# Kernel optimization log

Measured on AMD Instinct MI355X. Metric: run time of the kernel, lower is better.

Reference implementation:

```python
import jax, jax.numpy as jnp
import numpy as np

# ---- real Clebsch-Gordon tensors (Wigner 3j up to norm/sign) via equivariance null-space ----
def _su2_gens(l):
    m = np.arange(-l, l + 1)
    Lz = np.diag(m).astype(complex)
    c = np.sqrt(l * (l + 1) - m[:-1] * (m[:-1] + 1))
    Lp = np.zeros((2 * l + 1, 2 * l + 1), complex)
    Lp[np.arange(1, 2 * l + 1), np.arange(2 * l)] = c
    Lm = Lp.conj().T
    return (Lp + Lm) / 2, (Lp - Lm) / 2j, Lz

def _q_real(l):
    # complex -> real spherical-harmonic change of basis
    Q = np.zeros((2 * l + 1, 2 * l + 1), complex)
    s2 = np.sqrt(2.0)
    for m in range(-l, l + 1):
        i = m + l
        if m == 0:
            Q[i, l] = 1.0
        elif m > 0:
            Q[i, l + m] = (-1.0) ** m / s2
            Q[i, l - m] = 1.0 / s2
        else:
            Q[i, l + m] = 1j / s2
            Q[i, l - m] = -1j * (-1.0) ** m / s2
    return Q

def _real_gens(l):
    Q = _q_real(l)
    return [np.real(Q @ (1j * L) @ Q.conj().T) for L in _su2_gens(l)]

_CG = {}
def clebsch_gordon(l1, l2, l3):
    key = (l1, l2, l3)
    if key not in _CG:
        n1, n2, n3 = 2 * l1 + 1, 2 * l2 + 1, 2 * l3 + 1
        G = [_real_gens(l) for l in (l1, l2, l3)]
        rows = []
        for a in range(3):
            rows.append(np.kron(G[0][a], np.eye(n2 * n3))
                        + np.kron(np.eye(n1), np.kron(G[1][a], np.eye(n3)))
                        + np.kron(np.eye(n1 * n2), G[2][a]))
        _, s, Vh = np.linalg.svd(np.concatenate(rows, 0))
        v = Vh[-1]  # unique invariant vector (unit norm)
        if v[np.argmax(np.abs(v))] < 0:
            v = -v
        _CG[key] = v.reshape(n1, n2, n3).astype(np.float32)
    return _CG[key]

# ---- static irreps configuration (mul, degree l, parity p) ----
TP_L = [(32, 0, 1), (32, 1, -1)]
TP_R = [(32, 0, 1), (32, 1, -1)]
IRREPS_IN = [(128, 0, 1), (128, 1, -1), (128, 1, 1), (128, 2, 1)]
B = 8192
D_IN = sum(m * (2 * l + 1) for m, l, _ in IRREPS_IN)  # 1536

def _key(l, p):
    return f"{l}{'e' if p == 1 else 'o'}"

def _build_out_irreps():
    mul, order = {}, []
    for ml, ll, pl in TP_L:
        for mr, lr, pr in TP_R:
            p = pl * pr
            for l in range(abs(ll - lr), ll + lr + 1):
                k = _key(l, p)
                if k not in mul:
                    mul[k] = 0
                    order.append((l, p))
                mul[k] += ml * mr
    return [(mul[_key(l, p)], l, p) for (l, p) in order]

IRREPS_OUT = _build_out_irreps()  # [(2048,0,1),(2048,1,-1),(1024,1,1),(1024,2,1)]

def _build_schedule():
    # replicates the original's tail-consuming slice logic per (pair, output irrep)
    starts, off = [], 0
    for mul, l, p in IRREPS_OUT:
        starts.append(off)
        off += mul * (2 * l + 1)
    rem = {_key(l, p): mul for mul, l, p in IRREPS_OUT}
    sched = []
    for ml, ll, pl in TP_L:
        for mr, lr, pr in TP_R:
            mul = ml * mr
            terms = []
            for i, (mo, l, p) in enumerate(IRREPS_OUT):
                if p != pl * pr or not (abs(ll - lr) <= l <= ll + lr):
                    continue
                k = _key(l, p)
                stop = starts[i] + rem[k] * (2 * l + 1)
                start = stop - mul * (2 * l + 1)
                rem[k] -= mul
                terms.append((start, stop, l, clebsch_gordon(ll, lr, l)))
            sched.append((ml, ll, mr, lr, terms))
    assert all(v == 0 for v in rem.values())
    return sched, off

SCHEDULE, D_OUT = _build_schedule()  # D_OUT == 16384

def setup_inputs() -> dict:
    key = jax.random.key(0)
    ks = jax.random.split(key, 5)
    x = jax.random.normal(ks[0], (B, D_IN), jnp.float32)
    w_0e = jax.random.normal(ks[1], (128, 2048), jnp.float32) / np.sqrt(128.0)
    w_1o = jax.random.normal(ks[2], (128, 2048), jnp.float32) / np.sqrt(128.0)
    w_1e = jax.random.normal(ks[3], (128, 1024), jnp.float32) / np.sqrt(128.0)
    w_2e = jax.random.normal(ks[4], (128, 1024), jnp.float32) / np.sqrt(128.0)
    return {"x": x, "w_0e": w_0e, "w_1o": w_1o, "w_1e": w_1e, "w_2e": w_2e}

def _linear(x, ws):
    # e3nn-style PointwiseLinear: mix multiplicities within each irrep type
    in_off, off = {}, 0
    for m, l, p in IRREPS_IN:
        in_off[_key(l, p)] = (off, m)
        off += m * (2 * l + 1)
    outs = []
    for (mo, l, p), w in zip(IRREPS_OUT, ws):
        o, mi = in_off[_key(l, p)]
        d = 2 * l + 1
        xi = x[:, o:o + mi * d].reshape(-1, mi, d)  # [B, mul_in, 2l+1]
        yo = jnp.einsum('bui,uv->bvi', xi, w)       # [B, mul_out, 2l+1]
        outs.append(yo.reshape(xi.shape[0], mo * d))
    return jnp.concatenate(outs, axis=1)  # [B, D_OUT]

def reference(x, w_0e, w_1o, w_1e, w_2e):
    y = _linear(x, (w_0e, w_1o, w_1e, w_2e))
    blocks = []
    for ml, ll, mr, lr, terms in SCHEDULE:
        acc = None
        for start, stop, l, cg in terms:
            a = y[:, start:stop].reshape(-1, ml, mr, 2 * l + 1)  # [B,mul_l,mul_r,2l+1]
            t = jnp.einsum('bmni,lri->bmlnr', a, jnp.asarray(cg))
            acc = t if acc is None else acc + t  # [B,mul_l,2ll+1,mul_r,2lr+1]
        blocks.append(acc.reshape(acc.shape[0], -1))
    return jnp.concatenate(blocks, axis=1)  # [B, 16384]
```

## Files before the change

### kernel.cpp

```cpp
#include <hip/hip_runtime.h>


typedef __attribute__((ext_vector_type(8))) __bf16 bf16x8;
typedef __attribute__((ext_vector_type(8))) unsigned short u16x8;
typedef __attribute__((ext_vector_type(4))) float f32x4;

#define A_V8_TOTAL (12 * 512 * 4 * 64)
#define B_V8_TOTAL (384 * 4 * 64)
#define P_STRIDE   (512 * 4 * 64)
#define WS_NEED_BYTES ((size_t)(A_V8_TOTAL + B_V8_TOTAL) * 16)

__device__ __forceinline__ unsigned short f2bf(float f) {
  unsigned u = __builtin_bit_cast(unsigned, f);
  u = (u + 0x7FFFu + ((u >> 16) & 1u)) >> 16;
  return (unsigned short)u;
}

__device__ __forceinline__ f32x4 mfma16(bf16x8 a, bf16x8 b, f32x4 c) {
  return __builtin_amdgcn_mfma_f32_16x16x32_bf16(a, b, c, 0, 0, 0);
}
__device__ __forceinline__ bf16x8 asbf(u16x8 v) { return __builtin_bit_cast(bf16x8, v); }
__device__ __forceinline__ void stnt(float* p, float v) { __builtin_nontemporal_store(v, p); }

__device__ __forceinline__ void gload_lds16(const void* g, void* s) {
  __builtin_amdgcn_global_load_lds((const __attribute__((address_space(1))) void*)g,
                                   (__attribute__((address_space(3))) void*)s, 16, 0, 0);
}

__global__ __launch_bounds__(256) void prep_kernel(
    const float* __restrict__ x, const float* __restrict__ w0e,
    const float* __restrict__ w1o, const float* __restrict__ w1e,
    const float* __restrict__ w2e, u16x8* __restrict__ ws) {
  int t = blockIdx.x * 256 + threadIdx.x;
  if (t < A_V8_TOTAL) {
    int l = t & 63;
    int kb = (t >> 6) & 3;
    int mt = (t >> 8) & 511;
    int p = t >> 17;
    int m = mt * 16 + (l & 15);
    int k0 = kb * 32 + (l >> 4) * 8;
    int base, d, comp;
    if (p == 0)      { base = 0;   d = 1; comp = 0;     }
    else if (p < 4)  { base = 128; d = 3; comp = p - 1; }
    else if (p < 7)  { base = 512; d = 3; comp = p - 4; }
    else             { base = 896; d = 5; comp = p - 7; }
    const float* xr = x + (size_t)m * 1536 + base + comp + k0 * d;
    u16x8 v;
#pragma unroll
    for (int e = 0; e < 8; ++e) v[e] = f2bf(xr[e * d]);
    ws[t] = v;
  } else {
    int tb = t - A_V8_TOTAL;
    if (tb >= B_V8_TOTAL) return;
    int l = tb & 63;
    int kb = (tb >> 6) & 3;
    int ci = tb >> 8;
    const float* w; int N, v0;
    if (ci < 128)      { w = w0e; N = 2048; v0 = ci * 16;         }
    else if (ci < 256) { w = w1o; N = 2048; v0 = (ci - 128) * 16; }
    else if (ci < 320) { w = w1e; N = 1024; v0 = (ci - 256) * 16; }
    else               { w = w2e; N = 1024; v0 = (ci - 320) * 16; }
    int n = v0 + (l & 15);
    int k0 = kb * 32 + (l >> 4) * 8;
    u16x8 v;
#pragma unroll
    for (int e = 0; e < 8; ++e) v[e] = f2bf(w[(size_t)(k0 + e) * N + n]);
    ws[A_V8_TOTAL + tb] = v;
  }
}

__global__ __launch_bounds__(256) void tp_main(const u16x8* __restrict__ ws,
                                               float* __restrict__ out) {
  __shared__ __align__(16) u16x8 Ash[2][1536];
  const int tid = threadIdx.x;
  const int l = tid & 63;
  const int wv = tid >> 6;
  const int bid = blockIdx.x;
  const int logical = (bid & 7) * 1024 + (bid >> 3);
  const int mt2 = logical >> 5;
  const int vt = ((logical & 31) << 2) | wv;
  const int l15 = l & 15, lhi = l >> 4;
  const u16x8* Ap = ws;
  const u16x8* Bp = ws + A_V8_TOTAL;
  const bool isL = (logical & 31) < 16;
  const int nstage = isL ? 6 : 2;

  const float c3  = 0.57735026918962576f;
  const float c6  = 0.40824829046386302f;
  const float c10 = 0.31622776601683794f;
  const float c30 = 0.18257418583505537f;

  auto stageA = [&](int kb, int buf) {
    for (int i = 0; i < nstage; ++i) {
      const int e = i * 256 + tid;
      const int p = e >> 7, mfi = (e >> 6) & 1;
      const u16x8* src = Ap + (size_t)p * P_STRIDE +
                         (((((mt2 << 1) | mfi) << 2) + kb) << 6) + (e & 63);
      gload_lds16(src, &Ash[buf][i * 256 + (tid & 192)]);
    }
  };

  stageA(0, 0);

  if (isL) {
    f32x4 acc[2][12];
#pragma unroll
    for (int mf = 0; mf < 2; ++mf)
#pragma unroll
      for (int p = 0; p < 12; ++p) acc[mf][p] = (f32x4)(0.0f);

    const int ci0 = vt, ci1 = 128 + vt, ci2 = 256 + vt, ci3 = 320 + vt;
    int buf = 0;
#pragma unroll
    for (int kb = 0; kb < 4; ++kb) {
      __syncthreads();
      if (kb < 3) stageA(kb + 1, buf ^ 1);
      bf16x8 b0 = asbf(Bp[((ci0 << 2) + kb) * 64 + l]);
      bf16x8 b1 = asbf(Bp[((ci1 << 2) + kb) * 64 + l]);
      bf16x8 b2 = asbf(Bp[((ci2 << 2) + kb) * 64 + l]);
      bf16x8 b3 = asbf(Bp[((ci3 << 2) + kb) * 64 + l]);
#pragma unroll
      for (int mf = 0; mf < 2; ++mf) {
        const u16x8* af = &Ash[buf][mf * 64 + l];
        acc[mf][0]  = mfma16(asbf(af[0 * 128]),  b0, acc[mf][0]);
        acc[mf][1]  = mfma16(asbf(af[1 * 128]),  b1, acc[mf][1]);
        acc[mf][2]  = mfma16(asbf(af[2 * 128]),  b1, acc[mf][2]);
        acc[mf][3]  = mfma16(asbf(af[3 * 128]),  b1, acc[mf][3]);
        acc[mf][4]  = mfma16(asbf(af[4 * 128]),  b2, acc[mf][4]);
        acc[mf][5]  = mfma16(asbf(af[5 * 128]),  b2, acc[mf][5]);
        acc[mf][6]  = mfma16(asbf(af[6 * 128]),  b2, acc[mf][6]);
        acc[mf][7]  = mfma16(asbf(af[7 * 128]),  b3, acc[mf][7]);
        acc[mf][8]  = mfma16(asbf(af[8 * 128]),  b3, acc[mf][8]);
        acc[mf][9]  = mfma16(asbf(af[9 * 128]),  b3, acc[mf][9]);
        acc[mf][10] = mfma16(asbf(af[10 * 128]), b3, acc[mf][10]);
        acc[mf][11] = mfma16(asbf(af[11 * 128]), b3, acc[mf][11]);
      }
      buf ^= 1;
    }
    const int v5 = vt >> 1;
    const int v31 = ((vt & 1) << 4) | l15;
#pragma unroll
    for (int mf = 0; mf < 2; ++mf) {
#pragma unroll
      for (int j = 0; j < 4; ++j) {
        const int m = mt2 * 32 + mf * 16 + lhi * 4 + j;
        float* orow = out + (size_t)m * 16384;
        float* oc = orow + 4096 + v5 * 96 + v31;
        stnt(oc + 0,  acc[mf][1][j] * c3);
        stnt(oc + 32, acc[mf][2][j] * c3);
        stnt(oc + 64, acc[mf][3][j] * c3);
        const float s  = acc[mf][0][j] * c3;
        const float e0 = acc[mf][4][j], e1 = acc[mf][5][j], e2 = acc[mf][6][j];
        const float q0 = acc[mf][7][j], q1 = acc[mf][8][j];
        const float q2 = acc[mf][9][j], q3 = acc[mf][10][j], q4 = acc[mf][11][j];
        float* od = orow + 7168 + v5 * 288 + v31 * 3;
        stnt(od + 0,   s - q2 * c30 - q4 * c10);
        stnt(od + 1,   -e2 * c6 + q1 * c10);
        stnt(od + 2,   e1 * c6 + q0 * c10);
        stnt(od + 96,  e2 * c6 + q1 * c10);
        stnt(od + 97,  s + 2.0f * q2 * c30);
        stnt(od + 98,  -e0 * c6 + q3 * c10);
        stnt(od + 192, -e1 * c6 + q0 * c10);
        stnt(od + 193, e0 * c6 + q3 * c10);
        stnt(od + 194, s - q2 * c30 + q4 * c10);
      }
    }
  } else {
    const int vtp = vt - 64;
    f32x4 acc[2][4];
#pragma unroll
    for (int mf = 0; mf < 2; ++mf)
#pragma unroll
      for (int p = 0; p < 4; ++p) acc[mf][p] = (f32x4)(0.0f);

    const int ci0 = 64 + vtp, ci1 = 192 + vtp;
    int buf = 0;
#pragma unroll
    for (int kb = 0; kb < 4; ++kb) {
      __syncthreads();
      if (kb < 3) stageA(kb + 1, buf ^ 1);
      bf16x8 b0 = asbf(Bp[((ci0 << 2) + kb) * 64 + l]);
      bf16x8 b1 = asbf(Bp[((ci1 << 2) + kb) * 64 + l]);
#pragma unroll
      for (int mf = 0; mf < 2; ++mf) {
        const u16x8* af = &Ash[buf][mf * 64 + l];
        acc[mf][0] = mfma16(asbf(af[0 * 128]), b0, acc[mf][0]);
        acc[mf][1] = mfma16(asbf(af[1 * 128]), b1, acc[mf][1]);
        acc[mf][2] = mfma16(asbf(af[2 * 128]), b1, acc[mf][2]);
        acc[mf][3] = mfma16(asbf(af[3 * 128]), b1, acc[mf][3]);
      }
      buf ^= 1;
    }
    const int vp = vtp * 16 + l15;
#pragma unroll
    for (int mf = 0; mf < 2; ++mf) {
#pragma unroll
      for (int j = 0; j < 4; ++j) {
        const int m = mt2 * 32 + mf * 16 + lhi * 4 + j;
        float* orow = out + (size_t)m * 16384;
        stnt(orow + vp, acc[mf][0][j]);
        float* ob = orow + 1024 + vp * 3;
        stnt(ob + 0, acc[mf][1][j] * c3);
        stnt(ob + 1, acc[mf][2][j] * c3);
        stnt(ob + 2, acc[mf][3][j] * c3);
      }
    }
  }
}

extern "C" void kernel_launch(void* const* d_in, const int* in_sizes, int n_in,
                              void* d_out, int out_size, void* d_ws, size_t ws_size,
                              hipStream_t stream) {
  if (ws_size < WS_NEED_BYTES) return;
  const float* x   = (const float*)d_in[0];
  const float* w0e = (const float*)d_in[1];
  const float* w1o = (const float*)d_in[2];
  const float* w1e = (const float*)d_in[3];
  const float* w2e = (const float*)d_in[4];
  u16x8* ws = (u16x8*)d_ws;
  float* out = (float*)d_out;

  prep_kernel<<<6528, 256, 0, stream>>>(x, w0e, w1o, w1e, w2e, ws);
  tp_main<<<8192, 256, 0, stream>>>(ws, out);
}
```

Before: 147.4 us.

## Give each small-output wave two column tiles and shrink the grid

Blocks that handle the lighter output sections (the 0e/1o parts) now compute two column tiles per wave instead of one. Each A fragment loaded from LDS is reused across both tiles, and the grid drops from 8192 to 6144 blocks with a new block-to-tile mapping. The B-fragment global loads are also moved ahead of the async A staging so they are issued earlier. The cost is more accumulator registers in that branch, and the heavy and light blocks are now less evenly balanced.

```diff
diff --git a/kernel.cpp b/kernel.cpp
--- a/kernel.cpp
+++ b/kernel.cpp
@@ -76,13 +76,13 @@
   const int l = tid & 63;
   const int wv = tid >> 6;
   const int bid = blockIdx.x;
-  const int logical = (bid & 7) * 1024 + (bid >> 3);
-  const int mt2 = logical >> 5;
-  const int vt = ((logical & 31) << 2) | wv;
+  const int logical = (bid & 7) * 768 + (bid >> 3);
+  const int mt2 = logical / 24;
+  const int sub = logical - mt2 * 24;
   const int l15 = l & 15, lhi = l >> 4;
   const u16x8* Ap = ws;
   const u16x8* Bp = ws + A_V8_TOTAL;
-  const bool isL = (logical & 31) < 16;
+  const bool isL = sub < 16;
   const int nstage = isL ? 6 : 2;
 
   const float c3  = 0.57735026918962576f;
@@ -103,6 +103,7 @@
   stageA(0, 0);
 
   if (isL) {
+    const int vt = sub * 4 + wv;
     f32x4 acc[2][12];
 #pragma unroll
     for (int mf = 0; mf < 2; ++mf)
@@ -114,11 +115,11 @@
 #pragma unroll
     for (int kb = 0; kb < 4; ++kb) {
       __syncthreads();
-      if (kb < 3) stageA(kb + 1, buf ^ 1);
       bf16x8 b0 = asbf(Bp[((ci0 << 2) + kb) * 64 + l]);
       bf16x8 b1 = asbf(Bp[((ci1 << 2) + kb) * 64 + l]);
       bf16x8 b2 = asbf(Bp[((ci2 << 2) + kb) * 64 + l]);
       bf16x8 b3 = asbf(Bp[((ci3 << 2) + kb) * 64 + l]);
+      if (kb < 3) stageA(kb + 1, buf ^ 1);
 #pragma unroll
       for (int mf = 0; mf < 2; ++mf) {
         const u16x8* af = &Ash[buf][mf * 64 + l];
@@ -166,43 +167,59 @@
       }
     }
   } else {
-    const int vtp = vt - 64;
-    f32x4 acc[2][4];
+    const int hq = (sub - 16) * 4 + wv;
+    f32x4 acc[2][2][4];
 #pragma unroll
     for (int mf = 0; mf < 2; ++mf)
 #pragma unroll
-      for (int p = 0; p < 4; ++p) acc[mf][p] = (f32x4)(0.0f);
-
-    const int ci0 = 64 + vtp, ci1 = 192 + vtp;
+      for (int vs = 0; vs < 2; ++vs)
+#pragma unroll
+        for (int p = 0; p < 4; ++p) acc[mf][vs][p] = (f32x4)(0.0f);
+
     int buf = 0;
 #pragma unroll
     for (int kb = 0; kb < 4; ++kb) {
       __syncthreads();
+      bf16x8 b0[2], b1[2];
+#pragma unroll
+      for (int vs = 0; vs < 2; ++vs) {
+        const int vtp = hq * 2 + vs;
+        b0[vs] = asbf(Bp[(((64 + vtp)  << 2) + kb) * 64 + l]);
+        b1[vs] = asbf(Bp[(((192 + vtp) << 2) + kb) * 64 + l]);
+      }
       if (kb < 3) stageA(kb + 1, buf ^ 1);
-      bf16x8 b0 = asbf(Bp[((ci0 << 2) + kb) * 64 + l]);
-      bf16x8 b1 = asbf(Bp[((ci1 << 2) + kb) * 64 + l]);
 #pragma unroll
       for (int mf = 0; mf < 2; ++mf) {
         const u16x8* af = &Ash[buf][mf * 64 + l];
-        acc[mf][0] = mfma16(asbf(af[0 * 128]), b0, acc[mf][0]);
-        acc[mf][1] = mfma16(asbf(af[1 * 128]), b1, acc[mf][1]);
-        acc[mf][2] = mfma16(asbf(af[2 * 128]), b1, acc[mf][2]);
-        acc[mf][3] = mfma16(asbf(af[3 * 128]), b1, acc[mf][3]);
+        const bf16x8 a0 = asbf(af[0 * 128]);
+        const bf16x8 a1 = asbf(af[1 * 128]);
+        const bf16x8 a2 = asbf(af[2 * 128]);
+        const bf16x8 a3 = asbf(af[3 * 128]);
+#pragma unroll
+        for (int vs = 0; vs < 2; ++vs) {
+          acc[mf][vs][0] = mfma16(a0, b0[vs], acc[mf][vs][0]);
+          acc[mf][vs][1] = mfma16(a1, b1[vs], acc[mf][vs][1]);
+          acc[mf][vs][2] = mfma16(a2, b1[vs], acc[mf][vs][2]);
+          acc[mf][vs][3] = mfma16(a3, b1[vs], acc[mf][vs][3]);
+        }
       }
       buf ^= 1;
     }
-    const int vp = vtp * 16 + l15;
-#pragma unroll
-    for (int mf = 0; mf < 2; ++mf) {
-#pragma unroll
-      for (int j = 0; j < 4; ++j) {
-        const int m = mt2 * 32 + mf * 16 + lhi * 4 + j;
-        float* orow = out + (size_t)m * 16384;
-        stnt(orow + vp, acc[mf][0][j]);
-        float* ob = orow + 1024 + vp * 3;
-        stnt(ob + 0, acc[mf][1][j] * c3);
-        stnt(ob + 1, acc[mf][2][j] * c3);
-        stnt(ob + 2, acc[mf][3][j] * c3);
+#pragma unroll
+    for (int vs = 0; vs < 2; ++vs) {
+      const int vp = (hq * 2 + vs) * 16 + l15;
+#pragma unroll
+      for (int mf = 0; mf < 2; ++mf) {
+#pragma unroll
+        for (int j = 0; j < 4; ++j) {
+          const int m = mt2 * 32 + mf * 16 + lhi * 4 + j;
+          float* orow = out + (size_t)m * 16384;
+          stnt(orow + vp, acc[mf][vs][0][j]);
+          float* ob = orow + 1024 + vp * 3;
+          stnt(ob + 0, acc[mf][vs][1][j] * c3);
+          stnt(ob + 1, acc[mf][vs][2][j] * c3);
+          stnt(ob + 2, acc[mf][vs][3][j] * c3);
+        }
       }
     }
   }
@@ -221,5 +238,5 @@
   float* out = (float*)d_out;
 
   prep_kernel<<<6528, 256, 0, stream>>>(x, w0e, w1o, w1e, w2e, ws);
-  tp_main<<<8192, 256, 0, stream>>>(ws, out);
-}
+  tp_main<<<6144, 256, 0, stream>>>(ws, out);
+}
```

Result: slower. 151.7 us (+2.9%).
